# Kernel optimization log

Measured on AMD Instinct MI355X. Metric: run time of the kernel, lower is better.

The kernel has to match this reference:

```python
import jax, jax.numpy as jnp
import numpy as np

B, A, M, NCLS = 8, 100000, 100, 80
EPS = 1e-4


def setup_inputs() -> dict:
    key = jax.random.key(0)
    k1, k2, k3, k4, k5, k6, k7 = jax.random.split(key, 7)
    # predictions: [B, 4+1+classes, A]
    dt = jax.random.normal(k1, (B, 5 + NCLS, A), dtype=jnp.float32)
    # gt: [B, M, 5] = (x1, y1, w, h, class in 1..NCLS); padded entries are still
    # valid positive boxes so logs are finite (they are masked out of the loss).
    xy = jax.random.uniform(k2, (B, M, 2), minval=0.0, maxval=600.0)
    wh = jax.random.uniform(k3, (B, M, 2), minval=4.0, maxval=128.0)
    cls = jax.random.randint(k4, (B, M, 1), 1, NCLS + 1).astype(jnp.float32)
    gt = jnp.concatenate([xy, wh, cls], axis=-1)
    # anchors: [A, 4] in xyxy with positive width/height
    axy = jax.random.uniform(k5, (A, 2), minval=0.0, maxval=600.0)
    awh = jax.random.uniform(k6, (A, 2), minval=8.0, maxval=128.0)
    anchors = jnp.concatenate([axy, axy + awh], axis=-1)
    # assignment: -1 ignore, 0 background, k>=1 -> gt box index k-1
    assign_result = jax.random.randint(k7, (B, A), -1, M + 1).astype(jnp.int32)
    return {"dt": dt, "gt": gt, "anchors": anchors, "assign_result": assign_result}


def reference(dt, gt, anchors, assign_result):
    classes = dt.shape[1] - 5
    batch_size = dt.shape[0]
    af = assign_result.astype(jnp.float32)                  # [B, A]

    anch_w = anchors[:, 2] - anchors[:, 0]                  # [A]
    anch_h = anchors[:, 3] - anchors[:, 1]
    anch_x = anchors[:, 0] + 0.5 * anch_w
    anch_y = anchors[:, 1] + 0.5 * anch_h

    pos_cls = af >= -0.1                                    # assigned or background
    pos_box = af >= 0.9                                     # assigned to a gt box
    n_cls = pos_cls.sum(-1).astype(jnp.float32)             # [B]
    n_box = pos_box.sum(-1).astype(jnp.float32)

    # gather assigned gt annotation per anchor (clipped index; masked later)
    idx = jnp.clip(assign_result - 1, 0, gt.shape[1] - 1)   # [B, A]
    assigned = jnp.take_along_axis(gt, idx[..., None], axis=1)  # [B, A, 5]

    # ---- classification (BCE-style on objectness + one-hot class targets) ----
    obj_t = jnp.clip(af, 0.0, 1.0)                          # [B, A]
    oh = jax.nn.one_hot(assigned[..., 4].astype(jnp.int32) - 1, classes,
                        dtype=jnp.float32)                  # [B, A, C]
    oh = jnp.where(pos_box[..., None], oh, 0.0)
    tgt = jnp.concatenate([obj_t[..., None], oh], axis=-1)  # [B, A, 1+C]
    tgt = jnp.clip(tgt, EPS, 1.0 - EPS)
    dt_cls = jnp.clip(jnp.swapaxes(dt[:, 4:, :], 1, 2), EPS, 1.0 - EPS)  # [B, A, 1+C]
    cls_per = (-dt_cls * jnp.log(tgt) + (dt_cls - 1.0) * jnp.log(1.0 - tgt)).sum(-1)
    cls_loss = jnp.where(pos_cls, cls_per, 0.0).sum(-1) / jnp.maximum(n_cls, 1.0)

    ann_w = assigned[..., 2]
    ann_h = assigned[..., 3]
    ann_x = assigned[..., 0] + 0.5 * ann_w
    ann_y = assigned[..., 1] + 0.5 * ann_h
    tx = (ann_x - anch_x) / anch_w                          # [B, A]
    ty = (ann_y - anch_y) / anch_h
    tw = jnp.log(ann_w / anch_w)
    th = jnp.log(ann_h / anch_h)
    targets = jnp.stack([tx, ty, tw, th], axis=1)           # [B, 4, A]
    box_per = jnp.square(targets - dt[:, 0:4, :])           # [B, 4, A]
    box_sum = jnp.where(pos_box[:, None, :], box_per, 0.0).sum((1, 2))
    box_loss = jnp.where(n_box > 0, box_sum / jnp.maximum(n_box, 1.0), 0.0)

    return (box_loss.sum() + cls_loss.sum()) / batch_size
```

## Files before the change

kernel.cpp:

```cpp
#include <hip/hip_runtime.h>
#include <math.h>

constexpr int kB  = 8;
constexpr int kA  = 100000;
constexpr int kM  = 100;
constexpr int kCH = 85;
constexpr float kEPS = 1e-4f;

#define L0 (-9.210340371976182f)
#define L1 (-1.0000500033334732e-4f)

__device__ __forceinline__ float wave_reduce_f(float v) {
#pragma unroll
    for (int off = 32; off > 0; off >>= 1) v += __shfl_down(v, off, 64);
    return v;
}
__device__ __forceinline__ int wave_reduce_i(int v) {
#pragma unroll
    for (int off = 32; off > 0; off >>= 1) v += __shfl_down(v, off, 64);
    return v;
}

__global__ __launch_bounds__(256) void loss_main(
    const float* __restrict__ dt, const float* __restrict__ gt,
    const float* __restrict__ anchors, const int* __restrict__ assign,
    float* __restrict__ ws_f, int* __restrict__ ws_i)
{
    const int b = blockIdx.y;
    const int a = blockIdx.x * blockDim.x + threadIdx.x;

    float cls_c = 0.f, box_c = 0.f;
    int ncls_c = 0, nbox_c = 0;

    if (a < kA) {
        const int as = assign[b * kA + a];
        if (as >= 0) {
            const float* dp = dt + (size_t)b * kCH * kA + a;
            float P = 0.f;
#pragma unroll 9
            for (int c = 4; c < kCH; ++c) {
                float x = dp[(size_t)c * kA];
                x = fminf(fmaxf(x, kEPS), 1.0f - kEPS);
                P += x;
            }
            float per = (L1 - L0) * P - 81.0f * L1;
            if (as >= 1) {
                const int idx = min(as - 1, kM - 1);
                const float* g = gt + ((size_t)b * kM + idx) * 5;
                const float g0 = g[0], g1 = g[1], g2 = g[2], g3 = g[3];
                const int cls = (int)g[4];
                float p_obj = fminf(fmaxf(dp[(size_t)4 * kA], kEPS), 1.0f - kEPS);
                float p_cls = fminf(fmaxf(dp[(size_t)(4 + cls) * kA], kEPS), 1.0f - kEPS);
                per += (2.0f * (p_obj + p_cls) - 2.0f) * (L0 - L1);

                const float4 av = ((const float4*)anchors)[a];
                const float aw = av.z - av.x, ah = av.w - av.y;
                const float ax = av.x + 0.5f * aw, ay = av.y + 0.5f * ah;
                const float gx = g0 + 0.5f * g2, gy = g1 + 0.5f * g3;
                const float d0 = (gx - ax) / aw - dp[0];
                const float d1 = (gy - ay) / ah - dp[(size_t)1 * kA];
                const float d2 = logf(g2 / aw) - dp[(size_t)2 * kA];
                const float d3 = logf(g3 / ah) - dp[(size_t)3 * kA];
                box_c = d0 * d0 + d1 * d1 + d2 * d2 + d3 * d3;
                nbox_c = 1;
            }
            cls_c = per;
            ncls_c = 1;
        }
    }

    __shared__ float s_cls[4], s_box[4];
    __shared__ int   s_nc[4], s_nb[4];
    cls_c  = wave_reduce_f(cls_c);
    box_c  = wave_reduce_f(box_c);
    ncls_c = wave_reduce_i(ncls_c);
    nbox_c = wave_reduce_i(nbox_c);
    const int lane = threadIdx.x & 63, wid = threadIdx.x >> 6;
    if (lane == 0) { s_cls[wid] = cls_c; s_box[wid] = box_c; s_nc[wid] = ncls_c; s_nb[wid] = nbox_c; }
    __syncthreads();
    if (threadIdx.x == 0) {
        float cs = 0.f, bs = 0.f; int nc = 0, nb = 0;
#pragma unroll
        for (int w = 0; w < 4; ++w) { cs += s_cls[w]; bs += s_box[w]; nc += s_nc[w]; nb += s_nb[w]; }
        atomicAdd(&ws_f[b * 2 + 0], cs);
        atomicAdd(&ws_f[b * 2 + 1], bs);
        atomicAdd(&ws_i[b * 2 + 0], nc);
        atomicAdd(&ws_i[b * 2 + 1], nb);
    }
}

__global__ void loss_final(const float* __restrict__ ws_f,
                           const int* __restrict__ ws_i,
                           float* __restrict__ out)
{
    if (threadIdx.x == 0 && blockIdx.x == 0) {
        float tot = 0.f;
#pragma unroll
        for (int b = 0; b < kB; ++b) {
            const float cls_sum = ws_f[b * 2 + 0];
            const float box_sum = ws_f[b * 2 + 1];
            const float n_cls = (float)ws_i[b * 2 + 0];
            const float n_box = (float)ws_i[b * 2 + 1];
            const float cls_loss = cls_sum / fmaxf(n_cls, 1.0f);
            const float box_loss = (n_box > 0.f) ? box_sum / fmaxf(n_box, 1.0f) : 0.f;
            tot += cls_loss + box_loss;
        }
        out[0] = tot / (float)kB;
    }
}

extern "C" void kernel_launch(void* const* d_in, const int* in_sizes, int n_in,
                              void* d_out, int out_size, void* d_ws, size_t ws_size,
                              hipStream_t stream) {
    const float* dt      = (const float*)d_in[0];
    const float* gt      = (const float*)d_in[1];
    const float* anchors = (const float*)d_in[2];
    const int*   assign  = (const int*)d_in[3];
    float* out = (float*)d_out;

    float* ws_f = (float*)d_ws;
    int*   ws_i = (int*)(ws_f + 2 * kB);

    hipMemsetAsync(d_ws, 0, (2 * kB) * sizeof(float) + (2 * kB) * sizeof(int), stream);

    dim3 grid((kA + 255) / 256, kB);
    loss_main<<<grid, 256, 0, stream>>>(dt, gt, anchors, assign, ws_f, ws_i);
    loss_final<<<1, 64, 0, stream>>>(ws_f, ws_i, out);
}
```

Measured before the change: 404.7 us.

## Vectorize per-thread over 4 anchors and fuse final reduction via ticket

Each thread now handles four consecutive anchors using float4 loads across all 85 channels. It picks the target class probability in the streaming loop instead of issuing a separate gather, and preloads the box channels. The separate finalize kernel is replaced by a last-block ticket pattern inside the main kernel, which removes one launch. The cost is more registers per thread and a quarter as many threads. Almost all quadruples contain a non-ignored anchor, so nearly the full dt tensor is still read.

```diff
diff --git a/kernel.cpp b/kernel.cpp
--- a/kernel.cpp
+++ b/kernel.cpp
@@ -1,15 +1,19 @@
 #include <hip/hip_runtime.h>
 #include <math.h>
 
-constexpr int kB  = 8;
-constexpr int kA  = 100000;
-constexpr int kM  = 100;
-constexpr int kCH = 85;
+constexpr int kB   = 8;
+constexpr int kA   = 100000;
+constexpr int kM   = 100;
+constexpr int kCH  = 85;
+constexpr int kAd4 = kA / 4;
 constexpr float kEPS = 1e-4f;
 
 #define L0 (-9.210340371976182f)
 #define L1 (-1.0000500033334732e-4f)
 
+__device__ __forceinline__ float clipf(float x) {
+    return fminf(fmaxf(x, kEPS), 1.0f - kEPS);
+}
 __device__ __forceinline__ float wave_reduce_f(float v) {
 #pragma unroll
     for (int off = 32; off > 0; off >>= 1) v += __shfl_down(v, off, 64);
@@ -24,48 +28,85 @@
 __global__ __launch_bounds__(256) void loss_main(
     const float* __restrict__ dt, const float* __restrict__ gt,
     const float* __restrict__ anchors, const int* __restrict__ assign,
-    float* __restrict__ ws_f, int* __restrict__ ws_i)
+    float* __restrict__ ws_f, int* __restrict__ ws_i, int* __restrict__ ticket,
+    float* __restrict__ out, int nblocks)
 {
     const int b = blockIdx.y;
-    const int a = blockIdx.x * blockDim.x + threadIdx.x;
+    const int t = blockIdx.x * blockDim.x + threadIdx.x;
 
     float cls_c = 0.f, box_c = 0.f;
     int ncls_c = 0, nbox_c = 0;
 
-    if (a < kA) {
-        const int as = assign[b * kA + a];
-        if (as >= 0) {
-            const float* dp = dt + (size_t)b * kCH * kA + a;
-            float P = 0.f;
-#pragma unroll 9
-            for (int c = 4; c < kCH; ++c) {
-                float x = dp[(size_t)c * kA];
-                x = fminf(fmaxf(x, kEPS), 1.0f - kEPS);
-                P += x;
+    if (t < kAd4) {
+        const int a0 = t * 4;
+        const int4 as4 = ((const int4*)(assign + (size_t)b * kA))[t];
+        const int as[4] = {as4.x, as4.y, as4.z, as4.w};
+
+        if ((as[0] >= 0) | (as[1] >= 0) | (as[2] >= 0) | (as[3] >= 0)) {
+            int   tc[4];
+            float gx[4], gy[4], gw[4], gh[4];
+#pragma unroll
+            for (int j = 0; j < 4; ++j) {
+                int idx = as[j] - 1;
+                idx = idx < 0 ? 0 : (idx > kM - 1 ? kM - 1 : idx);
+                const float* g = gt + ((size_t)b * kM + idx) * 5;
+                gw[j] = g[2]; gh[j] = g[3];
+                gx[j] = g[0] + 0.5f * gw[j];
+                gy[j] = g[1] + 0.5f * gh[j];
+                tc[j] = (as[j] >= 1) ? (4 + (int)g[4]) : -1;
             }
-            float per = (L1 - L0) * P - 81.0f * L1;
-            if (as >= 1) {
-                const int idx = min(as - 1, kM - 1);
-                const float* g = gt + ((size_t)b * kM + idx) * 5;
-                const float g0 = g[0], g1 = g[1], g2 = g[2], g3 = g[3];
-                const int cls = (int)g[4];
-                float p_obj = fminf(fmaxf(dp[(size_t)4 * kA], kEPS), 1.0f - kEPS);
-                float p_cls = fminf(fmaxf(dp[(size_t)(4 + cls) * kA], kEPS), 1.0f - kEPS);
-                per += (2.0f * (p_obj + p_cls) - 2.0f) * (L0 - L1);
 
-                const float4 av = ((const float4*)anchors)[a];
-                const float aw = av.z - av.x, ah = av.w - av.y;
-                const float ax = av.x + 0.5f * aw, ay = av.y + 0.5f * ah;
-                const float gx = g0 + 0.5f * g2, gy = g1 + 0.5f * g3;
-                const float d0 = (gx - ax) / aw - dp[0];
-                const float d1 = (gy - ay) / ah - dp[(size_t)1 * kA];
-                const float d2 = logf(g2 / aw) - dp[(size_t)2 * kA];
-                const float d3 = logf(g3 / ah) - dp[(size_t)3 * kA];
-                box_c = d0 * d0 + d1 * d1 + d2 * d2 + d3 * d3;
-                nbox_c = 1;
+            const float* base = dt + (size_t)b * kCH * kA + a0;
+
+            float pr[4][4];
+#pragma unroll
+            for (int c = 0; c < 4; ++c)
+                *(float4*)pr[c] = *(const float4*)(base + (size_t)c * kA);
+
+            float P[4], pobj[4], pcls[4];
+            {
+                float x[4];
+                *(float4*)x = *(const float4*)(base + (size_t)4 * kA);
+#pragma unroll
+                for (int j = 0; j < 4; ++j) {
+                    float v = clipf(x[j]);
+                    P[j] = v; pobj[j] = v; pcls[j] = 0.f;
+                }
             }
-            cls_c = per;
-            ncls_c = 1;
+
+            const float* p = base + (size_t)5 * kA;
+#pragma unroll 8
+            for (int c = 5; c < kCH; ++c, p += kA) {
+                float x[4];
+                *(float4*)x = *(const float4*)p;
+#pragma unroll
+                for (int j = 0; j < 4; ++j) {
+                    float v = clipf(x[j]);
+                    P[j] += v;
+                    pcls[j] = (c == tc[j]) ? v : pcls[j];
+                }
+            }
+
+#pragma unroll
+            for (int j = 0; j < 4; ++j) {
+                if (as[j] >= 0) {
+                    float per = (L1 - L0) * P[j] - 81.0f * L1;
+                    if (as[j] >= 1) {
+                        per += (2.0f * (pobj[j] + pcls[j]) - 2.0f) * (L0 - L1);
+                        const float4 av = ((const float4*)anchors)[a0 + j];
+                        const float aw = av.z - av.x, ah = av.w - av.y;
+                        const float ax = av.x + 0.5f * aw, ay = av.y + 0.5f * ah;
+                        const float d0 = (gx[j] - ax) / aw - pr[0][j];
+                        const float d1 = (gy[j] - ay) / ah - pr[1][j];
+                        const float d2 = logf(gw[j] / aw) - pr[2][j];
+                        const float d3 = logf(gh[j] / ah) - pr[3][j];
+                        box_c += d0 * d0 + d1 * d1 + d2 * d2 + d3 * d3;
+                        nbox_c++;
+                    }
+                    cls_c += per;
+                    ncls_c++;
+                }
+            }
         }
     }
 
@@ -86,26 +127,26 @@
         atomicAdd(&ws_f[b * 2 + 1], bs);
         atomicAdd(&ws_i[b * 2 + 0], nc);
         atomicAdd(&ws_i[b * 2 + 1], nb);
-    }
-}
 
-__global__ void loss_final(const float* __restrict__ ws_f,
-                           const int* __restrict__ ws_i,
-                           float* __restrict__ out)
-{
-    if (threadIdx.x == 0 && blockIdx.x == 0) {
-        float tot = 0.f;
+        __threadfence();
+        const int old = atomicAdd(ticket, 1);
+        if (old == nblocks - 1) {
+            __threadfence();
+            const volatile float* vf = (const volatile float*)ws_f;
+            const volatile int*   vi = (const volatile int*)ws_i;
+            float tot = 0.f;
 #pragma unroll
-        for (int b = 0; b < kB; ++b) {
-            const float cls_sum = ws_f[b * 2 + 0];
-            const float box_sum = ws_f[b * 2 + 1];
-            const float n_cls = (float)ws_i[b * 2 + 0];
-            const float n_box = (float)ws_i[b * 2 + 1];
-            const float cls_loss = cls_sum / fmaxf(n_cls, 1.0f);
-            const float box_loss = (n_box > 0.f) ? box_sum / fmaxf(n_box, 1.0f) : 0.f;
-            tot += cls_loss + box_loss;
+            for (int bb = 0; bb < kB; ++bb) {
+                const float cls_sum = vf[bb * 2 + 0];
+                const float box_sum = vf[bb * 2 + 1];
+                const float n_cls = (float)vi[bb * 2 + 0];
+                const float n_box = (float)vi[bb * 2 + 1];
+                const float cls_loss = cls_sum / fmaxf(n_cls, 1.0f);
+                const float box_loss = (n_box > 0.f) ? box_sum / fmaxf(n_box, 1.0f) : 0.f;
+                tot += cls_loss + box_loss;
+            }
+            out[0] = tot / (float)kB;
         }
-        out[0] = tot / (float)kB;
     }
 }
 
@@ -118,12 +159,16 @@
     const int*   assign  = (const int*)d_in[3];
     float* out = (float*)d_out;
 
-    float* ws_f = (float*)d_ws;
-    int*   ws_i = (int*)(ws_f + 2 * kB);
+    float* ws_f   = (float*)d_ws;
+    int*   ws_i   = (int*)(ws_f + 2 * kB);
+    int*   ticket = ws_i + 2 * kB;
 
-    hipMemsetAsync(d_ws, 0, (2 * kB) * sizeof(float) + (2 * kB) * sizeof(int), stream);
+    hipMemsetAsync(d_ws, 0,
+                   (2 * kB) * sizeof(float) + (2 * kB) * sizeof(int) + sizeof(int),
+                   stream);
 
-    dim3 grid((kA + 255) / 256, kB);
-    loss_main<<<grid, 256, 0, stream>>>(dt, gt, anchors, assign, ws_f, ws_i);
-    loss_final<<<1, 64, 0, stream>>>(ws_f, ws_i, out);
+    dim3 grid((kAd4 + 255) / 256, kB);
+    const int nblocks = grid.x * grid.y;
+    loss_main<<<grid, 256, 0, stream>>>(dt, gt, anchors, assign,
+                                        ws_f, ws_i, ticket, out, nblocks);
 }
```

New measurement: 417.3 us. 3.1% more time.
